# Performance work log

Hardware: AMD Instinct MI355X
Metric: run time of the kernel (lower is better)

The kernel has to match this reference:

```python
import jax, jax.numpy as jnp
import numpy as np

B, HW, C = 32, 56, 128
WS, SS, NH = 7, 3, 4
HD = C // NH
SCALE = HD ** -0.5
NWIN = (HW // WS) ** 2  # 64 windows per image
N = WS * WS             # 49 tokens per window


def _build_constants():
    # relative position index [N, N] into flattened (13*13) bias table
    coords = np.stack(np.meshgrid(np.arange(WS), np.arange(WS), indexing='ij'))  # [2,7,7]
    cf = coords.reshape(2, -1)                       # [2,49]
    rel = cf[:, :, None] - cf[:, None, :]            # [2,49,49]
    rel = rel.transpose(1, 2, 0).copy()              # [49,49,2]
    rel[:, :, 0] += WS - 1
    rel[:, :, 1] += WS - 1
    rel[:, :, 0] *= 2 * WS - 1
    pos_index = rel.sum(-1)                          # [49,49]
    # shifted-window attention mask [nW, N, N]
    img = np.zeros((HW, HW))
    sl = (slice(0, -WS), slice(-WS, -SS), slice(-SS, None))
    cnt = 0
    for h in sl:
        for w in sl:
            img[h, w] = cnt
            cnt += 1
    mw = img.reshape(HW // WS, WS, HW // WS, WS).transpose(0, 2, 1, 3).reshape(NWIN, N)
    am = mw[:, None, :] - mw[:, :, None]             # unsqueeze(1) - unsqueeze(2)
    am = np.where(am != 0, -100.0, 0.0).astype(np.float32)
    return jnp.asarray(pos_index), jnp.asarray(am)

POS_INDEX, ATTN_MASK = _build_constants()


def _ln(x, w, b, eps=1e-5):
    mu = x.mean(-1, keepdims=True)
    var = ((x - mu) ** 2).mean(-1, keepdims=True)
    return (x - mu) * jax.lax.rsqrt(var + eps) * w + b


def setup_inputs() -> dict:
    key = jax.random.key(0)
    ks = jax.random.split(key, 10)
    s = 0.02
    return {
        'x': jax.random.normal(ks[0], (B, HW * HW, C), jnp.float32),
        'norm1_w': jnp.ones((C,), jnp.float32),
        'norm1_b': jnp.zeros((C,), jnp.float32),
        'qkv_w': jax.random.normal(ks[1], (C, 3 * C), jnp.float32) * s,
        'qkv_b': jax.random.normal(ks[2], (3 * C,), jnp.float32) * s,
        'proj_w': jax.random.normal(ks[3], (C, C), jnp.float32) * s,
        'proj_b': jax.random.normal(ks[4], (C,), jnp.float32) * s,
        'pos_bias_table': jax.random.normal(ks[5], (2 * WS - 1, 2 * WS - 1, NH), jnp.float32) * s,
        'mlp_w1': jax.random.normal(ks[6], (C, 4 * C), jnp.float32) * s,
        'mlp_b1': jnp.zeros((4 * C,), jnp.float32),
        'mlp_w2': jax.random.normal(ks[7], (4 * C, C), jnp.float32) * s,
        'mlp_b2': jnp.zeros((C,), jnp.float32),
        'norm2_w': jnp.ones((C,), jnp.float32),
        'norm2_b': jnp.zeros((C,), jnp.float32),
    }


def reference(x, norm1_w, norm1_b, qkv_w, qkv_b, proj_w, proj_b, pos_bias_table,
              mlp_w1, mlp_b1, mlp_w2, mlp_b2, norm2_w, norm2_b):
    G = HW // WS  # grid of windows per side
    Bw = B * NWIN
    shortcut = x
    y = _ln(x, norm1_w, norm1_b).reshape(B, HW, HW, C)
    # cyclic shift
    y = jnp.roll(y, (-SS, -SS), axis=(1, 2))
    # window partition -> [B*nW, 49, C]
    yw = y.reshape(B, G, WS, G, WS, C).transpose(0, 1, 3, 2, 4, 5).reshape(Bw, N, C)
    # qkv projection
    qkv = (yw @ qkv_w + qkv_b).reshape(Bw, N, 3, NH, HD).transpose(2, 0, 3, 1, 4)
    q, k, v = qkv[0] * SCALE, qkv[1], qkv[2]  # [Bw, NH, N, HD]
    attn = jnp.einsum('bhnd,bhmd->bhnm', q, k)
    # relative position bias [NH, N, N]
    bias = pos_bias_table.reshape(-1, NH)[POS_INDEX]  # [N,N,NH]
    attn = attn + bias.transpose(2, 0, 1)[None]
    # shift mask per window
    attn = attn.reshape(B, NWIN, NH, N, N) + ATTN_MASK[None, :, None]
    attn = jax.nn.softmax(attn.reshape(Bw, NH, N, N), axis=-1)
    out = jnp.einsum('bhnm,bhmd->bhnd', attn, v).transpose(0, 2, 1, 3).reshape(Bw, N, C)
    out = out @ proj_w + proj_b
    # window reverse
    out = out.reshape(B, G, G, WS, WS, C).transpose(0, 1, 3, 2, 4, 5).reshape(B, HW, HW, C)
    out = jnp.roll(out, (SS, SS), axis=(1, 2)).reshape(B, HW * HW, C)
    x = shortcut + out
    h = _ln(x, norm2_w, norm2_b)
    h = jax.nn.gelu(h @ mlp_w1 + mlp_b1, approximate=False) @ mlp_w2 + mlp_b2
    return x + h
```

## Files before the change

kernel.cpp:

```cpp
#include <hip/hip_runtime.h>
#include <hip/hip_bf16.h>

#define NTOK 100352
#define SCALE_Q 0.17677669529663687f

typedef __bf16 bf16x8 __attribute__((ext_vector_type(8)));
typedef float f32x4 __attribute__((ext_vector_type(4)));
struct bf2 { __hip_bfloat16 x, y; };

__device__ __forceinline__ int wt_to_tok(int wt) {
  int w = wt / 49, n = wt - w * 49;
  int b = w >> 6, wi = w & 63;
  int gh = wi >> 3, gw = wi & 7;
  int r = n / 7, c = n - r * 7;
  int hs = gh * 7 + r + 3; if (hs >= 56) hs -= 56;
  int ws = gw * 7 + c + 3; if (ws >= 56) ws -= 56;
  return (b * 56 + hs) * 56 + ws;
}

__device__ __forceinline__ float gelu_fast(float v) {
  float y = 0.7978845608028654f * (v + 0.044715f * v * v * v);
  float ay = fabsf(y);
  float e = __expf(-2.0f * ay);
  float t = (1.0f - e) / (1.0f + e);
  t = copysignf(t, y);
  return 0.5f * v * (1.0f + t);
}

__global__ __launch_bounds__(256) void prep_all(const float* __restrict__ qkvw,
                                                const float* __restrict__ projw,
                                                const float* __restrict__ w1,
                                                const float* __restrict__ w2,
                                                __hip_bfloat16* __restrict__ dst) {
  int i = blockIdx.x * 256 + threadIdx.x;
  float v;
  if (i < 49152) { int n = i >> 7, k = i & 127; v = qkvw[k * 384 + n]; }
  else if (i < 65536) { int j = i - 49152; int n = j >> 7, k = j & 127; v = projw[k * 128 + n]; }
  else if (i < 131072) { int j = i - 65536; int n = j >> 7, k = j & 127; v = w1[k * 512 + n]; }
  else { int j = i - 131072; int n = j / 512, k = j - n * 512; v = w2[k * 128 + n]; }
  dst[i] = __float2bfloat16(v);
}

__global__ __launch_bounds__(256) void ln1_apply(const float* __restrict__ x,
                                                 const float* __restrict__ nw,
                                                 const float* __restrict__ nb,
                                                 __hip_bfloat16* __restrict__ xn) {
  int wt = blockIdx.x * 4 + (threadIdx.x >> 6);
  int lane = threadIdx.x & 63;
  int tok = wt_to_tok(wt);
  float2 v = *(const float2*)(x + (size_t)tok * 128 + lane * 2);
  float s = v.x + v.y, ss = v.x * v.x + v.y * v.y;
#pragma unroll
  for (int off = 32; off; off >>= 1) {
    s += __shfl_xor(s, off);
    ss += __shfl_xor(ss, off);
  }
  float mu = s * (1.0f / 128.0f);
  float rstd = rsqrtf(ss * (1.0f / 128.0f) - mu * mu + 1e-5f);
  float2 wv = *(const float2*)(nw + lane * 2);
  float2 bv = *(const float2*)(nb + lane * 2);
  bf2 o;
  o.x = __float2bfloat16((v.x - mu) * rstd * wv.x + bv.x);
  o.y = __float2bfloat16((v.y - mu) * rstd * wv.y + bv.y);
  *(bf2*)(xn + (size_t)wt * 128 + lane * 2) = o;
}

__global__ __launch_bounds__(256) void attn_mfma(const __hip_bfloat16* __restrict__ qkv,
                                                 const float* __restrict__ ptab,
                                                 __hip_bfloat16* __restrict__ attnout) {
  __shared__ __align__(16) char lds[4 * 12288];
  const int tid = threadIdx.x;
  const int lane = tid & 63, h = tid >> 6;
  const int w = blockIdx.x;
  const int wi = w & 63, gh = wi >> 3, gw = wi & 7;
  char* Pl = lds + h * 12288;
  char* VTl = Pl + 8192;
  const int lxi = lane & 15, lq = lane >> 4, lg4 = (lane >> 4) * 4;

  const __hip_bfloat16* base = qkv + (size_t)w * 49 * 384 + h * 32;
  __hip_bfloat16* op = attnout + (size_t)w * 49 * 128 + h * 32;

  bf16x8 qa[4], kb[4];
#pragma unroll
  for (int mi = 0; mi < 4; ++mi) {
    int t = mi * 16 + lxi; if (t > 48) t = 48;
    qa[mi] = *(const bf16x8*)(base + (size_t)t * 384 + lq * 8);
    kb[mi] = *(const bf16x8*)(base + (size_t)t * 384 + 128 + lq * 8);
  }
  {
    union { bf16x8 v; __hip_bfloat16 e[8]; } vv[4];
    const __hip_bfloat16* vp = base + (size_t)(lane < 49 ? lane : 0) * 384 + 256;
#pragma unroll
    for (int q = 0; q < 4; ++q) vv[q].v = *(const bf16x8*)(vp + q * 8);
    __hip_bfloat16 z = __float2bfloat16(0.0f);
#pragma unroll
    for (int q = 0; q < 4; ++q)
#pragma unroll
      for (int e = 0; e < 8; ++e) {
        int d = q * 8 + e;
        __hip_bfloat16 val = (lane < 49) ? vv[q].e[e] : z;
        *(__hip_bfloat16*)(VTl + d * 128 + ((lane * 2) ^ ((d & 7) << 4))) = val;
      }
  }

  f32x4 s[4][4] = {};
#pragma unroll
  for (int mi = 0; mi < 4; ++mi)
#pragma unroll
    for (int ni = 0; ni < 4; ++ni)
      s[mi][ni] = __builtin_amdgcn_mfma_f32_16x16x32_bf16(qa[mi], kb[ni], s[mi][ni], 0, 0, 0);

  int rj[4], cj[4], cntj[4], jbad[4];
#pragma unroll
  for (int ni = 0; ni < 4; ++ni) {
    int jc = ni * 16 + lxi;
    jbad[ni] = (jc > 48);
    int jj = jbad[ni] ? 48 : jc;
    rj[ni] = jj / 7; cj[ni] = jj - rj[ni] * 7;
    int hj = gh * 7 + rj[ni], wj = gw * 7 + cj[ni];
    cntj[ni] = (hj < 49 ? 0 : (hj < 53 ? 3 : 6)) + (wj < 49 ? 0 : (wj < 53 ? 1 : 2));
  }
#pragma unroll
  for (int mi = 0; mi < 4; ++mi)
#pragma unroll
    for (int j = 0; j < 4; ++j) {
      int i = mi * 16 + lg4 + j; if (i > 48) i = 48;
      int ri = i / 7, ci = i - ri * 7;
      int hi_ = gh * 7 + ri, wi_ = gw * 7 + ci;
      int cnti = (hi_ < 49 ? 0 : (hi_ < 53 ? 3 : 6)) + (wi_ < 49 ? 0 : (wi_ < 53 ? 1 : 2));
#pragma unroll
      for (int ni = 0; ni < 4; ++ni) {
        float b = ptab[((ri - rj[ni] + 6) * 13 + (ci - cj[ni] + 6)) * 4 + h];
        float val = s[mi][ni][j] * SCALE_Q + b;
        if (cnti != cntj[ni]) val -= 100.0f;
        if (jbad[ni]) val = -1e30f;
        s[mi][ni][j] = val;
      }
    }

#pragma unroll
  for (int mi = 0; mi < 4; ++mi)
#pragma unroll
    for (int j = 0; j < 4; ++j) {
      float m = fmaxf(fmaxf(s[mi][0][j], s[mi][1][j]), fmaxf(s[mi][2][j], s[mi][3][j]));
#pragma unroll
      for (int off = 8; off; off >>= 1) m = fmaxf(m, __shfl_xor(m, off));
      float e[4], sum = 0.0f;
#pragma unroll
      for (int ni = 0; ni < 4; ++ni) { e[ni] = __expf(s[mi][ni][j] - m); sum += e[ni]; }
#pragma unroll
      for (int off = 8; off; off >>= 1) sum += __shfl_xor(sum, off);
      float inv = 1.0f / sum;
#pragma unroll
      for (int ni = 0; ni < 4; ++ni) s[mi][ni][j] = e[ni] * inv;
    }

#pragma unroll
  for (int mi = 0; mi < 4; ++mi)
#pragma unroll
    for (int j = 0; j < 4; ++j) {
      int row = mi * 16 + lg4 + j;
      int sw = (row & 7) << 4;
      char* prow = Pl + row * 128;
#pragma unroll
      for (int ni = 0; ni < 4; ++ni)
        *(__hip_bfloat16*)(prow + (((ni * 16 + lxi) * 2) ^ sw)) =
            __float2bfloat16(s[mi][ni][j]);
    }

  __syncthreads();

  f32x4 o[4][2] = {};
#pragma unroll
  for (int ks = 0; ks < 2; ++ks) {
    bf16x8 pa[4], vb[2];
#pragma unroll
    for (int mi = 0; mi < 4; ++mi) {
      int row = mi * 16 + lxi;
      pa[mi] = *(const bf16x8*)(Pl + row * 128 + ((ks * 64 + lq * 16) ^ ((row & 7) << 4)));
    }
#pragma unroll
    for (int ni = 0; ni < 2; ++ni) {
      int row = ni * 16 + lxi;
      vb[ni] = *(const bf16x8*)(VTl + row * 128 + ((ks * 64 + lq * 16) ^ ((row & 7) << 4)));
    }
#pragma unroll
    for (int mi = 0; mi < 4; ++mi)
#pragma unroll
      for (int ni = 0; ni < 2; ++ni)
        o[mi][ni] = __builtin_amdgcn_mfma_f32_16x16x32_bf16(pa[mi], vb[ni], o[mi][ni], 0, 0, 0);
  }

#pragma unroll
  for (int mi = 0; mi < 4; ++mi)
#pragma unroll
    for (int j = 0; j < 4; ++j) {
      int q = mi * 16 + lg4 + j;
      if (q < 49) {
#pragma unroll
        for (int ni = 0; ni < 2; ++ni)
          op[(size_t)q * 128 + ni * 16 + lxi] = __float2bfloat16(o[mi][ni][j]);
      }
    }
}

template<int EPI>
__global__ __launch_bounds__(256) void gemm_mfma(
    const __hip_bfloat16* __restrict__ A, int lda, int NB,
    const __hip_bfloat16* __restrict__ Wt,
    const float* __restrict__ bias,
    void* __restrict__ outv, int ldo,
    __hip_bfloat16* __restrict__ out2,
    const float* __restrict__ nw, const float* __restrict__ nb,
    const float* __restrict__ resf, const __hip_bfloat16* __restrict__ resb,
    int K)
{
  __shared__ __align__(16) char AsB[128 * 256];
  __shared__ __align__(16) char BsB[128 * 256];
  const int bid = blockIdx.x;
  const int xcd = bid & 7, tt = bid >> 3;
  const int nbk = tt % NB, mseq = tt / NB;
  const int m0 = (mseq * 8 + xcd) * 128, n0 = nbk * 128;
  const int tid = threadIdx.x;
  const int srow = tid >> 1;
  const int scol = (tid & 1) * 64;
  const int lane = tid & 63, wid = tid >> 6;
  const int wm = wid >> 1, wn = wid & 1;
  const int lrow = lane & 15, lq = lane >> 4;

  f32x4 acc[4][4] = {};

  for (int k0 = 0; k0 < K; k0 += 128) {
    {
      const char* ap = (const char*)A + ((size_t)(m0 + srow) * lda + k0 + scol) * 2;
      char* dst = AsB + srow * 256;
      int sw = (srow & 7) << 4;
#pragma unroll
      for (int t = 0; t < 8; ++t) {
        int4 raw = *(const int4*)(ap + t * 16);
        *(int4*)(dst + ((scol * 2 + t * 16) ^ sw)) = raw;
      }
    }
    {
      const char* bp = (const char*)Wt + ((size_t)(n0 + srow) * K + k0 + scol) * 2;
      char* dst = BsB + srow * 256;
      int sw = (srow & 7) << 4;
#pragma unroll
      for (int t = 0; t < 8; ++t) {
        int4 raw = *(const int4*)(bp + t * 16);
        *(int4*)(dst + ((scol * 2 + t * 16) ^ sw)) = raw;
      }
    }
    __syncthreads();
#pragma unroll
    for (int ks = 0; ks < 4; ++ks) {
      int kb = ks * 64 + lq * 16;
      bf16x8 af[4], bfr[4];
#pragma unroll
      for (int mi = 0; mi < 4; ++mi) {
        int r = wm * 64 + mi * 16 + lrow;
        af[mi] = *(const bf16x8*)(AsB + r * 256 + (kb ^ ((r & 7) << 4)));
      }
#pragma unroll
      for (int ni = 0; ni < 4; ++ni) {
        int r = wn * 64 + ni * 16 + lrow;
        bfr[ni] = *(const bf16x8*)(BsB + r * 256 + (kb ^ ((r & 7) << 4)));
      }
#pragma unroll
      for (int mi = 0; mi < 4; ++mi)
#pragma unroll
        for (int ni = 0; ni < 4; ++ni)
          acc[mi][ni] = __builtin_amdgcn_mfma_f32_16x16x32_bf16(af[mi], bfr[ni], acc[mi][ni], 0, 0, 0);
    }
    __syncthreads();
  }

  float bv[4];
#pragma unroll
  for (int ni = 0; ni < 4; ++ni) bv[ni] = bias[n0 + wn * 64 + ni * 16 + lrow];

  if (EPI == 4) {
    __hip_bfloat16* x2 = (__hip_bfloat16*)outv;
    float* redS = (float*)AsB;
    float* redQ = (float*)(AsB + 1024);
    float nwc[4], nbc[4];
#pragma unroll
    for (int ni = 0; ni < 4; ++ni) {
      int colg = wn * 64 + ni * 16 + lrow;
      nwc[ni] = nw[colg]; nbc[ni] = nb[colg];
    }
    int toks[4][4];
#pragma unroll
    for (int mi = 0; mi < 4; ++mi)
#pragma unroll
      for (int j = 0; j < 4; ++j) {
        int row = wm * 64 + mi * 16 + lq * 4 + j;
        int tok = wt_to_tok(m0 + row);
        toks[mi][j] = tok;
        float s = 0.0f, ss = 0.0f;
#pragma unroll
        for (int ni = 0; ni < 4; ++ni) {
          int colg = wn * 64 + ni * 16 + lrow;
          float val = acc[mi][ni][j] + bv[ni] + resf[(size_t)tok * 128 + colg];
          x2[(size_t)tok * 128 + colg] = __float2bfloat16(val);
          acc[mi][ni][j] = val;
          s += val; ss += val * val;
        }
#pragma unroll
        for (int off = 8; off; off >>= 1) {
          s += __shfl_xor(s, off);
          ss += __shfl_xor(ss, off);
        }
        if (lrow == 0) { redS[row * 2 + wn] = s; redQ[row * 2 + wn] = ss; }
      }
    __syncthreads();
#pragma unroll
    for (int mi = 0; mi < 4; ++mi)
#pragma unroll
      for (int j = 0; j < 4; ++j) {
        int row = wm * 64 + mi * 16 + lq * 4 + j;
        float s = redS[row * 2] + redS[row * 2 + 1];
        float ss = redQ[row * 2] + redQ[row * 2 + 1];
        float mu = s * (1.0f / 128.0f);
        float rstd = rsqrtf(ss * (1.0f / 128.0f) - mu * mu + 1e-5f);
        int tok = toks[mi][j];
#pragma unroll
        for (int ni = 0; ni < 4; ++ni) {
          int colg = wn * 64 + ni * 16 + lrow;
          float xnv = (acc[mi][ni][j] - mu) * rstd * nwc[ni] + nbc[ni];
          out2[(size_t)tok * 128 + colg] = __float2bfloat16(xnv);
        }
      }
    return;
  }

#pragma unroll
  for (int mi = 0; mi < 4; ++mi) {
#pragma unroll
    for (int j = 0; j < 4; ++j) {
      int rowg = m0 + wm * 64 + mi * 16 + lq * 4 + j;
#pragma unroll
      for (int ni = 0; ni < 4; ++ni) {
        int colg = n0 + wn * 64 + ni * 16 + lrow;
        float val = acc[mi][ni][j] + bv[ni];
        if (EPI == 0) {
          ((__hip_bfloat16*)outv)[(size_t)rowg * ldo + colg] = __float2bfloat16(val);
        } else if (EPI == 1) {
          ((__hip_bfloat16*)outv)[(size_t)rowg * ldo + colg] = __float2bfloat16(gelu_fast(val));
        } else {
          float r = __bfloat162float(resb[(size_t)rowg * 128 + colg]);
          ((float*)outv)[(size_t)rowg * 128 + colg] = val + r;
        }
      }
    }
  }
}

extern "C" void kernel_launch(void* const* d_in, const int* in_sizes, int n_in,
                              void* d_out, int out_size, void* d_ws, size_t ws_size,
                              hipStream_t stream) {
  (void)in_sizes; (void)n_in; (void)out_size; (void)ws_size;
  const float* x     = (const float*)d_in[0];
  const float* n1w   = (const float*)d_in[1];
  const float* n1b   = (const float*)d_in[2];
  const float* qkvw  = (const float*)d_in[3];
  const float* qkvb  = (const float*)d_in[4];
  const float* projw = (const float*)d_in[5];
  const float* projb = (const float*)d_in[6];
  const float* ptab  = (const float*)d_in[7];
  const float* w1    = (const float*)d_in[8];
  const float* b1    = (const float*)d_in[9];
  const float* w2    = (const float*)d_in[10];
  const float* b2    = (const float*)d_in[11];
  const float* n2w   = (const float*)d_in[12];
  const float* n2b   = (const float*)d_in[13];
  float* out = (float*)d_out;

  char* ws = (char*)d_ws;
  __hip_bfloat16* xn      = (__hip_bfloat16*)ws;
  __hip_bfloat16* qkv     = (__hip_bfloat16*)(ws + 25690112);
  __hip_bfloat16* attnout = (__hip_bfloat16*)(ws + 102760448);
  __hip_bfloat16* u       = (__hip_bfloat16*)(ws + 25690112);
  __hip_bfloat16* x2      = (__hip_bfloat16*)(ws + 128450560);
  __hip_bfloat16* x2n     = (__hip_bfloat16*)(ws + 154140672);
  __hip_bfloat16* wbase   = (__hip_bfloat16*)(ws + 179830784);
  __hip_bfloat16* qkvwT  = wbase;
  __hip_bfloat16* projwT = wbase + 49152;
  __hip_bfloat16* w1T    = wbase + 65536;
  __hip_bfloat16* w2T    = wbase + 131072;

  prep_all<<<768, 256, 0, stream>>>(qkvw, projw, w1, w2, wbase);
  ln1_apply<<<NTOK / 4, 256, 0, stream>>>(x, n1w, n1b, xn);
  gemm_mfma<0><<<784 * 3, 256, 0, stream>>>(xn, 128, 3, qkvwT, qkvb,
                                            qkv, 384, nullptr, nullptr, nullptr,
                                            nullptr, nullptr, 128);
  attn_mfma<<<2048, 256, 0, stream>>>(qkv, ptab, attnout);
  gemm_mfma<4><<<784, 256, 0, stream>>>(attnout, 128, 1, projwT, projb,
                                        x2, 128, x2n, n2w, n2b, x, nullptr, 128);
  gemm_mfma<1><<<784 * 4, 256, 0, stream>>>(x2n, 128, 4, w1T, b1,
                                            (void*)u, 512, nullptr, nullptr, nullptr,
                                            nullptr, nullptr, 128);
  gemm_mfma<3><<<784, 256, 0, stream>>>(u, 512, 1, w2T, b2,
                                        out, 128, nullptr, nullptr, nullptr,
                                        nullptr, x2, 512);
}
```

Before: 256.7 us.

## Fuse MLP fc1+GELU+fc2 into one kernel and read weights directly from global

Replaces the two MLP GEMM launches with a single fused kernel. Each block keeps a 128-token tile of normalized activations in shared memory, computes the 512-wide hidden layer in 128-column chunks with GELU into shared memory, and accumulates the fc2 output in registers before adding the residual. This removes the write and re-read of the large hidden activation buffer. Separately, the generic GEMM drops its shared-memory staging of weight tiles and loads weight fragments straight from global memory, relying on cache hits for the small weights and cutting LDS use, at the cost of uncoalesced global loads inside the MFMA loop.

```diff
diff --git a/kernel.cpp b/kernel.cpp
--- a/kernel.cpp
+++ b/kernel.cpp
@@ -7,6 +7,7 @@
 typedef __bf16 bf16x8 __attribute__((ext_vector_type(8)));
 typedef float f32x4 __attribute__((ext_vector_type(4)));
 struct bf2 { __hip_bfloat16 x, y; };
+struct __align__(8) bh4 { __hip_bfloat16 a, b, c, d; };
 
 __device__ __forceinline__ int wt_to_tok(int wt) {
   int w = wt / 49, n = wt - w * 49;
@@ -212,11 +213,10 @@
     void* __restrict__ outv, int ldo,
     __hip_bfloat16* __restrict__ out2,
     const float* __restrict__ nw, const float* __restrict__ nb,
-    const float* __restrict__ resf, const __hip_bfloat16* __restrict__ resb,
-    int K)
+    const float* __restrict__ resf, int K)
 {
   __shared__ __align__(16) char AsB[128 * 256];
-  __shared__ __align__(16) char BsB[128 * 256];
+  __shared__ float redS[256], redQ[256];
   const int bid = blockIdx.x;
   const int xcd = bid & 7, tt = bid >> 3;
   const int nbk = tt % NB, mseq = tt / NB;
@@ -241,16 +241,6 @@
         *(int4*)(dst + ((scol * 2 + t * 16) ^ sw)) = raw;
       }
     }
-    {
-      const char* bp = (const char*)Wt + ((size_t)(n0 + srow) * K + k0 + scol) * 2;
-      char* dst = BsB + srow * 256;
-      int sw = (srow & 7) << 4;
-#pragma unroll
-      for (int t = 0; t < 8; ++t) {
-        int4 raw = *(const int4*)(bp + t * 16);
-        *(int4*)(dst + ((scol * 2 + t * 16) ^ sw)) = raw;
-      }
-    }
     __syncthreads();
 #pragma unroll
     for (int ks = 0; ks < 4; ++ks) {
@@ -263,8 +253,8 @@
       }
 #pragma unroll
       for (int ni = 0; ni < 4; ++ni) {
-        int r = wn * 64 + ni * 16 + lrow;
-        bfr[ni] = *(const bf16x8*)(BsB + r * 256 + (kb ^ ((r & 7) << 4)));
+        int n = n0 + wn * 64 + ni * 16 + lrow;
+        bfr[ni] = *(const bf16x8*)(Wt + (size_t)n * K + k0 + ks * 32 + lq * 8);
       }
 #pragma unroll
       for (int mi = 0; mi < 4; ++mi)
@@ -281,8 +271,6 @@
 
   if (EPI == 4) {
     __hip_bfloat16* x2 = (__hip_bfloat16*)outv;
-    float* redS = (float*)AsB;
-    float* redQ = (float*)(AsB + 1024);
     float nwc[4], nbc[4];
 #pragma unroll
     for (int ni = 0; ni < 4; ++ni) {
@@ -343,17 +331,122 @@
       for (int ni = 0; ni < 4; ++ni) {
         int colg = n0 + wn * 64 + ni * 16 + lrow;
         float val = acc[mi][ni][j] + bv[ni];
-        if (EPI == 0) {
-          ((__hip_bfloat16*)outv)[(size_t)rowg * ldo + colg] = __float2bfloat16(val);
-        } else if (EPI == 1) {
-          ((__hip_bfloat16*)outv)[(size_t)rowg * ldo + colg] = __float2bfloat16(gelu_fast(val));
-        } else {
-          float r = __bfloat162float(resb[(size_t)rowg * 128 + colg]);
-          ((float*)outv)[(size_t)rowg * 128 + colg] = val + r;
-        }
-      }
-    }
-  }
+        ((__hip_bfloat16*)outv)[(size_t)rowg * ldo + colg] = __float2bfloat16(val);
+      }
+    }
+  }
+}
+
+__global__ __launch_bounds__(256) void mlp_fused(
+    const __hip_bfloat16* __restrict__ x2n,
+    const __hip_bfloat16* __restrict__ w1T,
+    const float* __restrict__ b1,
+    const __hip_bfloat16* __restrict__ w2T,
+    const float* __restrict__ b2,
+    const __hip_bfloat16* __restrict__ x2,
+    float* __restrict__ out)
+{
+  __shared__ __align__(16) char AsB[128 * 256];
+  __shared__ __align__(16) char Hs[128 * 256];
+  const int m0 = blockIdx.x * 128;
+  const int tid = threadIdx.x;
+  const int srow = tid >> 1, scol = (tid & 1) * 64;
+  const int lane = tid & 63, wid = tid >> 6;
+  const int wm = wid >> 1, wn = wid & 1;
+  const int lrow = lane & 15, lq = lane >> 4;
+
+  {
+    const char* ap = (const char*)x2n + ((size_t)(m0 + srow) * 128 + scol) * 2;
+    char* dst = AsB + srow * 256;
+    int sw = (srow & 7) << 4;
+#pragma unroll
+    for (int t = 0; t < 8; ++t) {
+      int4 raw = *(const int4*)(ap + t * 16);
+      *(int4*)(dst + ((scol * 2 + t * 16) ^ sw)) = raw;
+    }
+  }
+  __syncthreads();
+
+  f32x4 oacc[4][4] = {};
+
+  for (int c = 0; c < 4; ++c) {
+    f32x4 hacc[4][4] = {};
+#pragma unroll
+    for (int ks = 0; ks < 4; ++ks) {
+      int kb = ks * 64 + lq * 16;
+      bf16x8 wf[4], afr[4];
+#pragma unroll
+      for (int mi = 0; mi < 4; ++mi) {
+        int hd = c * 128 + wm * 64 + mi * 16 + lrow;
+        wf[mi] = *(const bf16x8*)(w1T + (size_t)hd * 128 + ks * 32 + lq * 8);
+      }
+#pragma unroll
+      for (int ni = 0; ni < 4; ++ni) {
+        int r = wn * 64 + ni * 16 + lrow;
+        afr[ni] = *(const bf16x8*)(AsB + r * 256 + (kb ^ ((r & 7) << 4)));
+      }
+#pragma unroll
+      for (int mi = 0; mi < 4; ++mi)
+#pragma unroll
+        for (int ni = 0; ni < 4; ++ni)
+          hacc[mi][ni] = __builtin_amdgcn_mfma_f32_16x16x32_bf16(wf[mi], afr[ni], hacc[mi][ni], 0, 0, 0);
+    }
+    __syncthreads();
+#pragma unroll
+    for (int mi = 0; mi < 4; ++mi) {
+      int hdb = wm * 64 + mi * 16 + lq * 4;
+      float b1v[4];
+#pragma unroll
+      for (int j = 0; j < 4; ++j) b1v[j] = b1[c * 128 + hdb + j];
+#pragma unroll
+      for (int ni = 0; ni < 4; ++ni) {
+        int m_ = wn * 64 + ni * 16 + lrow;
+        bh4 hv;
+        hv.a = __float2bfloat16(gelu_fast(hacc[mi][ni][0] + b1v[0]));
+        hv.b = __float2bfloat16(gelu_fast(hacc[mi][ni][1] + b1v[1]));
+        hv.c = __float2bfloat16(gelu_fast(hacc[mi][ni][2] + b1v[2]));
+        hv.d = __float2bfloat16(gelu_fast(hacc[mi][ni][3] + b1v[3]));
+        *(bh4*)(Hs + m_ * 256 + ((hdb * 2) ^ ((m_ & 7) << 4))) = hv;
+      }
+    }
+    __syncthreads();
+#pragma unroll
+    for (int ks = 0; ks < 4; ++ks) {
+      int kb = ks * 64 + lq * 16;
+      bf16x8 hf[4], w2f[4];
+#pragma unroll
+      for (int mi = 0; mi < 4; ++mi) {
+        int r = wm * 64 + mi * 16 + lrow;
+        hf[mi] = *(const bf16x8*)(Hs + r * 256 + (kb ^ ((r & 7) << 4)));
+      }
+#pragma unroll
+      for (int ni = 0; ni < 4; ++ni) {
+        int n = wn * 64 + ni * 16 + lrow;
+        w2f[ni] = *(const bf16x8*)(w2T + (size_t)n * 512 + c * 128 + ks * 32 + lq * 8);
+      }
+#pragma unroll
+      for (int mi = 0; mi < 4; ++mi)
+#pragma unroll
+        for (int ni = 0; ni < 4; ++ni)
+          oacc[mi][ni] = __builtin_amdgcn_mfma_f32_16x16x32_bf16(hf[mi], w2f[ni], oacc[mi][ni], 0, 0, 0);
+    }
+  }
+
+  float bv[4];
+#pragma unroll
+  for (int ni = 0; ni < 4; ++ni) bv[ni] = b2[wn * 64 + ni * 16 + lrow];
+#pragma unroll
+  for (int mi = 0; mi < 4; ++mi)
+#pragma unroll
+    for (int j = 0; j < 4; ++j) {
+      int row = m0 + wm * 64 + mi * 16 + lq * 4 + j;
+#pragma unroll
+      for (int ni = 0; ni < 4; ++ni) {
+        int col = wn * 64 + ni * 16 + lrow;
+        float r = __bfloat162float(x2[(size_t)row * 128 + col]);
+        out[(size_t)row * 128 + col] = oacc[mi][ni][j] + bv[ni] + r;
+      }
+    }
 }
 
 extern "C" void kernel_launch(void* const* d_in, const int* in_sizes, int n_in,
@@ -380,7 +473,6 @@
   __hip_bfloat16* xn      = (__hip_bfloat16*)ws;
   __hip_bfloat16* qkv     = (__hip_bfloat16*)(ws + 25690112);
   __hip_bfloat16* attnout = (__hip_bfloat16*)(ws + 102760448);
-  __hip_bfloat16* u       = (__hip_bfloat16*)(ws + 25690112);
   __hip_bfloat16* x2      = (__hip_bfloat16*)(ws + 128450560);
   __hip_bfloat16* x2n     = (__hip_bfloat16*)(ws + 154140672);
   __hip_bfloat16* wbase   = (__hip_bfloat16*)(ws + 179830784);
@@ -393,14 +485,9 @@
   ln1_apply<<<NTOK / 4, 256, 0, stream>>>(x, n1w, n1b, xn);
   gemm_mfma<0><<<784 * 3, 256, 0, stream>>>(xn, 128, 3, qkvwT, qkvb,
                                             qkv, 384, nullptr, nullptr, nullptr,
-                                            nullptr, nullptr, 128);
+                                            nullptr, 128);
   attn_mfma<<<2048, 256, 0, stream>>>(qkv, ptab, attnout);
   gemm_mfma<4><<<784, 256, 0, stream>>>(attnout, 128, 1, projwT, projb,
-                                        x2, 128, x2n, n2w, n2b, x, nullptr, 128);
-  gemm_mfma<1><<<784 * 4, 256, 0, stream>>>(x2n, 128, 4, w1T, b1,
-                                            (void*)u, 512, nullptr, nullptr, nullptr,
-                                            nullptr, nullptr, 128);
-  gemm_mfma<3><<<784, 256, 0, stream>>>(u, 512, 1, w2T, b2,
-                                        out, 128, nullptr, nullptr, nullptr,
-                                        nullptr, x2, 512);
-}
+                                        x2, 128, x2n, n2w, n2b, x, 128);
+  mlp_fused<<<784, 256, 0, stream>>>(x2n, w1T, b1, w2T, b2, x2, out);
+}
```

Result: no change. 252.3 us (-1.7%).

## Replace LDS-staged GEMMs with register-resident weights and persistent M-tile loops

Applied to the files above, without the earlier changes.

The shared-memory-staged GEMM is replaced by kernels that load A and B fragments straight from global memory into registers, with no LDS and no barriers in the main loop. For the K=128 GEMMs, each block keeps its 128-column weight slice in registers and loops over several M tiles, reusing the weights across tiles. The K=512 down-projection gets its own kernel that streams both operands from global memory per K step. This removes LDS traffic and synchronisation and cuts block count, but it adds register pressure and duplicate global loads across waves, and relies on L2 for operand reuse.

```diff
diff --git a/kernel.cpp b/kernel.cpp
--- a/kernel.cpp
+++ b/kernel.cpp
@@ -204,155 +204,182 @@
     }
 }
 
-template<int EPI>
-__global__ __launch_bounds__(256) void gemm_mfma(
-    const __hip_bfloat16* __restrict__ A, int lda, int NB,
+template<int NB, int T, int EPI>
+__global__ __launch_bounds__(256, 2) void gemm_mloop(
+    const __hip_bfloat16* __restrict__ A,
     const __hip_bfloat16* __restrict__ Wt,
     const float* __restrict__ bias,
     void* __restrict__ outv, int ldo,
     __hip_bfloat16* __restrict__ out2,
     const float* __restrict__ nw, const float* __restrict__ nb,
-    const float* __restrict__ resf, const __hip_bfloat16* __restrict__ resb,
-    int K)
+    const float* __restrict__ resf)
 {
-  __shared__ __align__(16) char AsB[128 * 256];
-  __shared__ __align__(16) char BsB[128 * 256];
+  __shared__ float redS[256], redQ[256];
   const int bid = blockIdx.x;
   const int xcd = bid & 7, tt = bid >> 3;
-  const int nbk = tt % NB, mseq = tt / NB;
-  const int m0 = (mseq * 8 + xcd) * 128, n0 = nbk * 128;
-  const int tid = threadIdx.x;
-  const int srow = tid >> 1;
-  const int scol = (tid & 1) * 64;
-  const int lane = tid & 63, wid = tid >> 6;
+  const int nbk = tt % NB, cseq = tt / NB;
+  const int chunk = cseq * 8 + xcd;
+  const int n0 = nbk * 128;
+  const int lane = threadIdx.x & 63, wid = threadIdx.x >> 6;
   const int wm = wid >> 1, wn = wid & 1;
-  const int lrow = lane & 15, lq = lane >> 4;
-
-  f32x4 acc[4][4] = {};
-
-  for (int k0 = 0; k0 < K; k0 += 128) {
-    {
-      const char* ap = (const char*)A + ((size_t)(m0 + srow) * lda + k0 + scol) * 2;
-      char* dst = AsB + srow * 256;
-      int sw = (srow & 7) << 4;
-#pragma unroll
-      for (int t = 0; t < 8; ++t) {
-        int4 raw = *(const int4*)(ap + t * 16);
-        *(int4*)(dst + ((scol * 2 + t * 16) ^ sw)) = raw;
-      }
-    }
-    {
-      const char* bp = (const char*)Wt + ((size_t)(n0 + srow) * K + k0 + scol) * 2;
-      char* dst = BsB + srow * 256;
-      int sw = (srow & 7) << 4;
-#pragma unroll
-      for (int t = 0; t < 8; ++t) {
-        int4 raw = *(const int4*)(bp + t * 16);
-        *(int4*)(dst + ((scol * 2 + t * 16) ^ sw)) = raw;
-      }
-    }
-    __syncthreads();
-#pragma unroll
-    for (int ks = 0; ks < 4; ++ks) {
-      int kb = ks * 64 + lq * 16;
-      bf16x8 af[4], bfr[4];
-#pragma unroll
-      for (int mi = 0; mi < 4; ++mi) {
-        int r = wm * 64 + mi * 16 + lrow;
-        af[mi] = *(const bf16x8*)(AsB + r * 256 + (kb ^ ((r & 7) << 4)));
-      }
-#pragma unroll
-      for (int ni = 0; ni < 4; ++ni) {
-        int r = wn * 64 + ni * 16 + lrow;
-        bfr[ni] = *(const bf16x8*)(BsB + r * 256 + (kb ^ ((r & 7) << 4)));
-      }
-#pragma unroll
-      for (int mi = 0; mi < 4; ++mi)
-#pragma unroll
-        for (int ni = 0; ni < 4; ++ni)
-          acc[mi][ni] = __builtin_amdgcn_mfma_f32_16x16x32_bf16(af[mi], bfr[ni], acc[mi][ni], 0, 0, 0);
-    }
-    __syncthreads();
-  }
-
+  const int lrow = lane & 15, lq = lane >> 4, lg4 = (lane >> 4) * 4;
+
+  bf16x8 breg[4][4];
+#pragma unroll
+  for (int ni = 0; ni < 4; ++ni) {
+    const __hip_bfloat16* bp = Wt + (size_t)(n0 + wn * 64 + ni * 16 + lrow) * 128 + lq * 8;
+#pragma unroll
+    for (int ks = 0; ks < 4; ++ks) breg[ni][ks] = *(const bf16x8*)(bp + ks * 32);
+  }
   float bv[4];
 #pragma unroll
   for (int ni = 0; ni < 4; ++ni) bv[ni] = bias[n0 + wn * 64 + ni * 16 + lrow];
-
+  float nwc[4], nbc[4];
   if (EPI == 4) {
-    __hip_bfloat16* x2 = (__hip_bfloat16*)outv;
-    float* redS = (float*)AsB;
-    float* redQ = (float*)(AsB + 1024);
-    float nwc[4], nbc[4];
 #pragma unroll
     for (int ni = 0; ni < 4; ++ni) {
       int colg = wn * 64 + ni * 16 + lrow;
       nwc[ni] = nw[colg]; nbc[ni] = nb[colg];
     }
-    int toks[4][4];
+  }
+
+#pragma unroll
+  for (int t = 0; t < T; ++t) {
+    int mt = chunk * T + t;
+    if (mt * 128 >= NTOK) break;
+    int m0 = mt * 128;
+
+    bf16x8 af[4][4];
+#pragma unroll
+    for (int mi = 0; mi < 4; ++mi) {
+      const __hip_bfloat16* ap = A + (size_t)(m0 + wm * 64 + mi * 16 + lrow) * 128 + lq * 8;
+#pragma unroll
+      for (int ks = 0; ks < 4; ++ks) af[mi][ks] = *(const bf16x8*)(ap + ks * 32);
+    }
+    f32x4 acc[4][4] = {};
+#pragma unroll
+    for (int ks = 0; ks < 4; ++ks)
+#pragma unroll
+      for (int mi = 0; mi < 4; ++mi)
+#pragma unroll
+        for (int ni = 0; ni < 4; ++ni)
+          acc[mi][ni] = __builtin_amdgcn_mfma_f32_16x16x32_bf16(af[mi][ks], breg[ni][ks], acc[mi][ni], 0, 0, 0);
+
+    if (EPI == 4) {
+      __hip_bfloat16* x2 = (__hip_bfloat16*)outv;
+      int toks[4][4];
+#pragma unroll
+      for (int mi = 0; mi < 4; ++mi)
+#pragma unroll
+        for (int j = 0; j < 4; ++j) {
+          int row = wm * 64 + mi * 16 + lq * 4 + j;
+          int tok = wt_to_tok(m0 + row);
+          toks[mi][j] = tok;
+          float s = 0.0f, ss = 0.0f;
+#pragma unroll
+          for (int ni = 0; ni < 4; ++ni) {
+            int colg = wn * 64 + ni * 16 + lrow;
+            float val = acc[mi][ni][j] + bv[ni] + resf[(size_t)tok * 128 + colg];
+            x2[(size_t)tok * 128 + colg] = __float2bfloat16(val);
+            acc[mi][ni][j] = val;
+            s += val; ss += val * val;
+          }
+#pragma unroll
+          for (int off = 8; off; off >>= 1) {
+            s += __shfl_xor(s, off);
+            ss += __shfl_xor(ss, off);
+          }
+          if (lrow == 0) { redS[row * 2 + wn] = s; redQ[row * 2 + wn] = ss; }
+        }
+      __syncthreads();
+#pragma unroll
+      for (int mi = 0; mi < 4; ++mi)
+#pragma unroll
+        for (int j = 0; j < 4; ++j) {
+          int row = wm * 64 + mi * 16 + lq * 4 + j;
+          float s = redS[row * 2] + redS[row * 2 + 1];
+          float ss = redQ[row * 2] + redQ[row * 2 + 1];
+          float mu = s * (1.0f / 128.0f);
+          float rstd = rsqrtf(ss * (1.0f / 128.0f) - mu * mu + 1e-5f);
+          int tok = toks[mi][j];
+#pragma unroll
+          for (int ni = 0; ni < 4; ++ni) {
+            int colg = wn * 64 + ni * 16 + lrow;
+            float xnv = (acc[mi][ni][j] - mu) * rstd * nwc[ni] + nbc[ni];
+            out2[(size_t)tok * 128 + colg] = __float2bfloat16(xnv);
+          }
+        }
+      if (t + 1 < T) __syncthreads();
+    } else {
+#pragma unroll
+      for (int mi = 0; mi < 4; ++mi)
+#pragma unroll
+        for (int j = 0; j < 4; ++j) {
+          int rowg = m0 + wm * 64 + mi * 16 + lq * 4 + j;
+#pragma unroll
+          for (int ni = 0; ni < 4; ++ni) {
+            int colg = n0 + wn * 64 + ni * 16 + lrow;
+            float val = acc[mi][ni][j] + bv[ni];
+            if (EPI == 1) val = gelu_fast(val);
+            ((__hip_bfloat16*)outv)[(size_t)rowg * ldo + colg] = __float2bfloat16(val);
+          }
+        }
+    }
+  }
+}
+
+template<int T>
+__global__ __launch_bounds__(256, 2) void gemm_k512(
+    const __hip_bfloat16* __restrict__ A,
+    const __hip_bfloat16* __restrict__ Wt,
+    const float* __restrict__ b2,
+    const __hip_bfloat16* __restrict__ x2,
+    float* __restrict__ out)
+{
+  const int bid = blockIdx.x;
+  const int xcd = bid & 7, cseq = bid >> 3;
+  const int chunk = cseq * 8 + xcd;
+  const int lane = threadIdx.x & 63, wid = threadIdx.x >> 6;
+  const int wm = wid >> 1, wn = wid & 1;
+  const int lrow = lane & 15, lq = lane >> 4;
+
+  float bv[4];
+#pragma unroll
+  for (int ni = 0; ni < 4; ++ni) bv[ni] = b2[wn * 64 + ni * 16 + lrow];
+
+#pragma unroll
+  for (int t = 0; t < T; ++t) {
+    int mt = chunk * T + t;
+    if (mt * 128 >= NTOK) break;
+    int m0 = mt * 128;
+    f32x4 acc[4][4] = {};
+#pragma unroll
+    for (int ks = 0; ks < 16; ++ks) {
+      bf16x8 af[4], bf_[4];
+#pragma unroll
+      for (int mi = 0; mi < 4; ++mi)
+        af[mi] = *(const bf16x8*)(A + (size_t)(m0 + wm * 64 + mi * 16 + lrow) * 512 + ks * 32 + lq * 8);
+#pragma unroll
+      for (int ni = 0; ni < 4; ++ni)
+        bf_[ni] = *(const bf16x8*)(Wt + (size_t)(wn * 64 + ni * 16 + lrow) * 512 + ks * 32 + lq * 8);
+#pragma unroll
+      for (int mi = 0; mi < 4; ++mi)
+#pragma unroll
+        for (int ni = 0; ni < 4; ++ni)
+          acc[mi][ni] = __builtin_amdgcn_mfma_f32_16x16x32_bf16(af[mi], bf_[ni], acc[mi][ni], 0, 0, 0);
+    }
 #pragma unroll
     for (int mi = 0; mi < 4; ++mi)
 #pragma unroll
       for (int j = 0; j < 4; ++j) {
-        int row = wm * 64 + mi * 16 + lq * 4 + j;
-        int tok = wt_to_tok(m0 + row);
-        toks[mi][j] = tok;
-        float s = 0.0f, ss = 0.0f;
+        int row = m0 + wm * 64 + mi * 16 + lq * 4 + j;
 #pragma unroll
         for (int ni = 0; ni < 4; ++ni) {
-          int colg = wn * 64 + ni * 16 + lrow;
-          float val = acc[mi][ni][j] + bv[ni] + resf[(size_t)tok * 128 + colg];
-          x2[(size_t)tok * 128 + colg] = __float2bfloat16(val);
-          acc[mi][ni][j] = val;
-          s += val; ss += val * val;
-        }
-#pragma unroll
-        for (int off = 8; off; off >>= 1) {
-          s += __shfl_xor(s, off);
-          ss += __shfl_xor(ss, off);
-        }
-        if (lrow == 0) { redS[row * 2 + wn] = s; redQ[row * 2 + wn] = ss; }
-      }
-    __syncthreads();
-#pragma unroll
-    for (int mi = 0; mi < 4; ++mi)
-#pragma unroll
-      for (int j = 0; j < 4; ++j) {
-        int row = wm * 64 + mi * 16 + lq * 4 + j;
-        float s = redS[row * 2] + redS[row * 2 + 1];
-        float ss = redQ[row * 2] + redQ[row * 2 + 1];
-        float mu = s * (1.0f / 128.0f);
-        float rstd = rsqrtf(ss * (1.0f / 128.0f) - mu * mu + 1e-5f);
-        int tok = toks[mi][j];
-#pragma unroll
-        for (int ni = 0; ni < 4; ++ni) {
-          int colg = wn * 64 + ni * 16 + lrow;
-          float xnv = (acc[mi][ni][j] - mu) * rstd * nwc[ni] + nbc[ni];
-          out2[(size_t)tok * 128 + colg] = __float2bfloat16(xnv);
+          int col = wn * 64 + ni * 16 + lrow;
+          float r = __bfloat162float(x2[(size_t)row * 128 + col]);
+          out[(size_t)row * 128 + col] = acc[mi][ni][j] + bv[ni] + r;
         }
       }
-    return;
-  }
-
-#pragma unroll
-  for (int mi = 0; mi < 4; ++mi) {
-#pragma unroll
-    for (int j = 0; j < 4; ++j) {
-      int rowg = m0 + wm * 64 + mi * 16 + lq * 4 + j;
-#pragma unroll
-      for (int ni = 0; ni < 4; ++ni) {
-        int colg = n0 + wn * 64 + ni * 16 + lrow;
-        float val = acc[mi][ni][j] + bv[ni];
-        if (EPI == 0) {
-          ((__hip_bfloat16*)outv)[(size_t)rowg * ldo + colg] = __float2bfloat16(val);
-        } else if (EPI == 1) {
-          ((__hip_bfloat16*)outv)[(size_t)rowg * ldo + colg] = __float2bfloat16(gelu_fast(val));
-        } else {
-          float r = __bfloat162float(resb[(size_t)rowg * 128 + colg]);
-          ((float*)outv)[(size_t)rowg * 128 + colg] = val + r;
-        }
-      }
-    }
   }
 }
 
@@ -391,16 +418,12 @@
 
   prep_all<<<768, 256, 0, stream>>>(qkvw, projw, w1, w2, wbase);
   ln1_apply<<<NTOK / 4, 256, 0, stream>>>(x, n1w, n1b, xn);
-  gemm_mfma<0><<<784 * 3, 256, 0, stream>>>(xn, 128, 3, qkvwT, qkvb,
-                                            qkv, 384, nullptr, nullptr, nullptr,
-                                            nullptr, nullptr, 128);
+  gemm_mloop<3, 4, 0><<<600, 256, 0, stream>>>(xn, qkvwT, qkvb,
+                                               qkv, 384, nullptr, nullptr, nullptr, nullptr);
   attn_mfma<<<2048, 256, 0, stream>>>(qkv, ptab, attnout);
-  gemm_mfma<4><<<784, 256, 0, stream>>>(attnout, 128, 1, projwT, projb,
-                                        x2, 128, x2n, n2w, n2b, x, nullptr, 128);
-  gemm_mfma<1><<<784 * 4, 256, 0, stream>>>(x2n, 128, 4, w1T, b1,
-                                            (void*)u, 512, nullptr, nullptr, nullptr,
-                                            nullptr, nullptr, 128);
-  gemm_mfma<3><<<784, 256, 0, stream>>>(u, 512, 1, w2T, b2,
-                                        out, 128, nullptr, nullptr, nullptr,
-                                        nullptr, x2, 512);
-}
+  gemm_mloop<1, 2, 4><<<392, 256, 0, stream>>>(attnout, projwT, projb,
+                                               x2, 128, x2n, n2w, n2b, x);
+  gemm_mloop<4, 4, 1><<<800, 256, 0, stream>>>(x2n, w1T, b1,
+                                               (void*)u, 512, nullptr, nullptr, nullptr, nullptr);
+  gemm_k512<2><<<392, 256, 0, stream>>>(u, w2T, b2, x2, out);
+}
```

Result: slower. 296.4 us (+15.5%).
